# Kernel optimization log

Hardware: AMD Instinct MI355X
Metric: run time of the kernel (lower is better)

## Reference

```python
import jax, jax.numpy as jnp
import numpy as np

N_NODES = 100000
N_EDGES = 1600000
IN_CH, HID_CH, OUT_CH = 128, 64, 32


def setup_inputs() -> dict:
    key = jax.random.key(0)
    k1, k2, k3, k4 = jax.random.split(key, 4)
    x = jax.random.normal(k1, (N_NODES, IN_CH), dtype=jnp.float32)
    edge_index = jax.random.randint(k2, (2, N_EDGES), 0, N_NODES, dtype=jnp.int32)
    # Glorot-ish scaling like PyG's GCNConv init
    W1 = jax.random.normal(k3, (IN_CH, HID_CH), dtype=jnp.float32) / np.sqrt(IN_CH)
    b1 = jnp.zeros((HID_CH,), dtype=jnp.float32)
    W2 = jax.random.normal(k4, (HID_CH, OUT_CH), dtype=jnp.float32) / np.sqrt(HID_CH)
    b2 = jnp.zeros((OUT_CH,), dtype=jnp.float32)
    return {"x": x, "edge_index": edge_index, "W1": W1, "b1": b1, "W2": W2, "b2": b2}


def reference(x, edge_index, W1, b1, W2, b2):
    # PyG GCNConv semantics: add self-loops, symmetric deg^{-1/2} normalization,
    # linear transform, scatter-add aggregation to destination nodes, add bias.
    N = x.shape[0]
    loops = jnp.arange(N, dtype=edge_index.dtype)
    src = jnp.concatenate([edge_index[0], loops])  # [E+N]
    dst = jnp.concatenate([edge_index[1], loops])  # [E+N]

    deg = jax.ops.segment_sum(jnp.ones_like(src, dtype=x.dtype), dst, num_segments=N)
    dis = jnp.where(deg > 0, jax.lax.rsqrt(jnp.maximum(deg, 1.0)), 0.0)  # deg^{-1/2}
    norm = (dis[src] * dis[dst])[:, None]  # [E+N, 1]

    def gcn_conv(h, W, b):
        h = h @ W                                   # [N, C_out]
        msgs = h[src] * norm                        # gather + scale, [E+N, C_out]
        return jax.ops.segment_sum(msgs, dst, num_segments=N) + b

    h = jax.nn.relu(gcn_conv(x, W1, b1))
    # dropout is identity in eval mode (training=False)
    return gcn_conv(h, W2, b2)
```

## Files before the change

### kernel.cpp

```cpp
#include <hip/hip_runtime.h>
#include <hip/hip_bf16.h>

#define IN_CH 128
#define HID_CH 64
#define OUT_CH 32
#define EPB 2048
#define MAXB 512

typedef unsigned short ushort_t;
typedef __attribute__((ext_vector_type(8))) short short8;
typedef __attribute__((ext_vector_type(4))) float float4v;
typedef __attribute__((ext_vector_type(4))) float fx4;
typedef __attribute__((ext_vector_type(4))) unsigned ux4;
using half8 = __attribute__((ext_vector_type(8))) _Float16;

static __device__ __forceinline__ ushort_t f2bf(float f) {
    unsigned u = __float_as_uint(f);
    unsigned r = (u + 0x7fff + ((u >> 16) & 1)) >> 16;
    return (ushort_t)r;
}
static __device__ __forceinline__ float bf_lo(unsigned u) { return __uint_as_float(u << 16); }
static __device__ __forceinline__ float bf_hi(unsigned u) { return __uint_as_float(u & 0xffff0000u); }

static __device__ __forceinline__ unsigned f2h2(float lo, float hi) {
    union { _Float16 h[2]; unsigned u; } v;
    v.h[0] = (_Float16)lo;
    v.h[1] = (_Float16)hi;
    return v.u;
}
static __device__ __forceinline__ unsigned pkh(float a, float b) {
    auto p = __builtin_amdgcn_cvt_pkrtz(a, b);
    union { decltype(p) h; unsigned u; } v;
    v.h = p;
    return v.u;
}


__global__ __launch_bounds__(256) void k_partition(const int* __restrict__ src,
                                                   const int* __restrict__ dst,
                                                   int* __restrict__ gcursor,
                                                   unsigned* __restrict__ pairs,
                                                   int E, int nbk, int cap, int PB,
                                                   const float* __restrict__ W1,
                                                   const float* __restrict__ W2,
                                                   unsigned* __restrict__ wsW) {
    __shared__ int lhist[MAXB];
    __shared__ int lbase[MAXB];
    __shared__ int lcur[MAXB];
    const int tid = threadIdx.x;

    if (blockIdx.x >= PB) {
        int s = (blockIdx.x - PB) * 256 + tid;
        if (s < 1024) {
            int lane = s & 63;
            int nt = (s >> 6) & 3;
            int kc = s >> 8;
            int c = nt * 16 + (lane & 15);
            int k0 = kc * 32 + (lane >> 4) * 8;
            unsigned o[4];
#pragma unroll
            for (int d = 0; d < 4; ++d) {
                unsigned lo = f2bf(W1[(k0 + 2 * d) * 64 + c]);
                unsigned hi = f2bf(W1[(k0 + 2 * d + 1) * 64 + c]);
                o[d] = lo | (hi << 16);
            }
            ((uint4*)wsW)[s] = make_uint4(o[0], o[1], o[2], o[3]);
        } else {
            int q = s - 1024;
            int lane = q & 63;
            int f = q >> 6;
            int c = (f & 1) * 16 + (lane & 15);
            int k0 = (f >> 1) * 32 + (lane >> 4) * 8;
            unsigned o[4];
#pragma unroll
            for (int d = 0; d < 4; ++d)
                o[d] = f2h2(W2[(k0 + 2 * d) * 32 + c], W2[(k0 + 2 * d + 1) * 32 + c]);
            ((uint4*)wsW)[1024 + q] = make_uint4(o[0], o[1], o[2], o[3]);
        }
        return;
    }

    for (int b = tid; b < nbk; b += 256) { lhist[b] = 0; lcur[b] = 0; }
    __syncthreads();
    int s[8], d[8];
    const int e0 = blockIdx.x * EPB;
#pragma unroll
    for (int j = 0; j < 8; ++j) {
        int e = e0 + j * 256 + tid;
        if (e < E) {
            s[j] = src[e];
            d[j] = dst[e];
            atomicAdd(&lhist[d[j] >> 8], 1);
        } else {
            d[j] = -1;
        }
    }
    __syncthreads();
    for (int b = tid; b < nbk; b += 256)
        lbase[b] = lhist[b] ? atomicAdd(&gcursor[b], lhist[b]) : 0;
    __syncthreads();
#pragma unroll
    for (int j = 0; j < 8; ++j) {
        if (d[j] >= 0) {
            int b = d[j] >> 8;
            int loc = atomicAdd(&lcur[b], 1);
            int idx = lbase[b] + loc;
            if (idx < cap)
                pairs[(long long)b * cap + idx] = ((unsigned)s[j] << 8) | (unsigned)(d[j] & 255);
        }
    }
}


__global__ __launch_bounds__(256) void k_bucket_build(const unsigned* __restrict__ pairs,
                                                      const int* __restrict__ gcursor,
                                                      int* __restrict__ rowptr,
                                                      int* __restrict__ col,
                                                      float* __restrict__ dis,
                                                      unsigned* __restrict__ h1d,
                                                      int cap, int N) {
    __shared__ int lc[256];
    __shared__ int ls[256];
    __shared__ int lcur[256];
    const int b = blockIdx.x, tid = threadIdx.x;

    if (b == 0 && tid < 32)
        h1d[(long long)(tid >> 4) * (N + 1) * 16 + (long long)N * 16 + (tid & 15)] = 0;

    int ga = min(gcursor[2 * tid], cap);
    int gb = min(gcursor[2 * tid + 1], cap);
    ls[tid] = ga + gb;
    __syncthreads();
    for (int off = 1; off < 256; off <<= 1) {
        int val = (tid >= off) ? ls[tid - off] : 0;
        __syncthreads();
        ls[tid] += val;
        __syncthreads();
    }
    const int p = b >> 1;
    const int base = (p ? ls[p - 1] : 0) + ((b & 1) ? min(gcursor[b - 1], cap) : 0);
    const int total = ls[255];
    __syncthreads();
    if (b == 0 && tid == 0) rowptr[N] = total;

    lc[tid] = 0;
    __syncthreads();
    const int cnt = min(gcursor[b], cap);
    const unsigned* pp = pairs + (long long)b * cap;
    for (int i = tid; i < cnt; i += 256) atomicAdd(&lc[pp[i] & 255], 1);
    __syncthreads();
    const int v = lc[tid];
    ls[tid] = v;
    __syncthreads();
    for (int off = 1; off < 256; off <<= 1) {
        int val = (tid >= off) ? ls[tid - off] : 0;
        __syncthreads();
        ls[tid] += val;
        __syncthreads();
    }
    const int excl = ls[tid] - v;
    const int row = b * 256 + tid;
    if (row < N) {
        rowptr[row] = base + excl;
        dis[row] = rsqrtf((float)(v + 1));
    }
    lcur[tid] = base + excl;
    __syncthreads();
    for (int i = tid; i < cnt; i += 256) {
        unsigned pk = pp[i];
        int pos = atomicAdd(&lcur[pk & 255], 1);
        col[pos] = (int)(pk >> 8);
    }
}


__global__ __launch_bounds__(256) void k_mm1(const float* __restrict__ X,
                                             const unsigned* __restrict__ wsW,
                                             const float* __restrict__ dis,
                                             ushort_t* __restrict__ H, int N) {
    const int tid = threadIdx.x;
    const int wv = tid >> 6, lane = tid & 63;
    const int quad = lane >> 4, n16 = lane & 15;
    const int rowbase = blockIdx.x * 64 + wv * 16;
    const int myrow = rowbase + n16;
    const bool rok = (myrow < N);

    float4v acc0 = {}, acc1 = {}, acc2 = {}, acc3 = {};

#pragma unroll
    for (int kc = 0; kc < 4; ++kc) {
        float4 xa = make_float4(0.f, 0.f, 0.f, 0.f), xb = xa;
        if (rok) {
            const float4* p = (const float4*)(X + (long long)myrow * 128 + kc * 32 + quad * 8);
            xa = p[0];
            xb = p[1];
        }
        unsigned pk[4];
        pk[0] = (unsigned)f2bf(xa.x) | ((unsigned)f2bf(xa.y) << 16);
        pk[1] = (unsigned)f2bf(xa.z) | ((unsigned)f2bf(xa.w) << 16);
        pk[2] = (unsigned)f2bf(xb.x) | ((unsigned)f2bf(xb.y) << 16);
        pk[3] = (unsigned)f2bf(xb.z) | ((unsigned)f2bf(xb.w) << 16);
        short8 a;
        a[0] = (short)(pk[0] & 0xffff); a[1] = (short)(pk[0] >> 16);
        a[2] = (short)(pk[1] & 0xffff); a[3] = (short)(pk[1] >> 16);
        a[4] = (short)(pk[2] & 0xffff); a[5] = (short)(pk[2] >> 16);
        a[6] = (short)(pk[3] & 0xffff); a[7] = (short)(pk[3] >> 16);

        const short8* wb = (const short8*)wsW;
        short8 b0 = wb[(kc * 4 + 0) * 64 + lane];
        short8 b1 = wb[(kc * 4 + 1) * 64 + lane];
        short8 b2 = wb[(kc * 4 + 2) * 64 + lane];
        short8 b3 = wb[(kc * 4 + 3) * 64 + lane];

        acc0 = __builtin_amdgcn_mfma_f32_16x16x32_bf16(a, b0, acc0, 0, 0, 0);
        acc1 = __builtin_amdgcn_mfma_f32_16x16x32_bf16(a, b1, acc1, 0, 0, 0);
        acc2 = __builtin_amdgcn_mfma_f32_16x16x32_bf16(a, b2, acc2, 0, 0, 0);
        acc3 = __builtin_amdgcn_mfma_f32_16x16x32_bf16(a, b3, acc3, 0, 0, 0);
    }

    const long long hb1 = (long long)(N + 1) * 32;
#pragma unroll
    for (int i = 0; i < 4; ++i) {
        int row = rowbase + quad * 4 + i;
        if (row < N) {
            float dr = dis[row];
            long long o = (long long)row * 32 + n16;
            H[o]            = f2bf(dr * acc0[i]);
            H[o + 16]       = f2bf(dr * acc1[i]);
            H[hb1 + o]      = f2bf(dr * acc2[i]);
            H[hb1 + o + 16] = f2bf(dr * acc3[i]);
        }
    }
}


__global__ __launch_bounds__(256, 8) void k_gather1h(const unsigned* __restrict__ h,
                                                     const int* __restrict__ rowptr,
                                                     const int* __restrict__ col,
                                                     const float* __restrict__ dis,
                                                     const float* __restrict__ b1,
                                                     unsigned* __restrict__ z, int N) {
    const int tid = threadIdx.x;
    const int wv = tid >> 6, lane = tid & 63;
    const int t = lane & 3, g = lane >> 2;
    const int xcd = blockIdx.x & 7;
    const int hf = xcd >> 2;
    const int pb = ((blockIdx.x >> 3) << 2) | (xcd & 3);
    const int nwh = ((gridDim.x >> 3) << 2) * 4;

    const uint4* h4 = (const uint4*)h + (long long)hf * (N + 1) * 4;
    ux4* zp = (ux4*)z + (long long)hf * (N + 1) * 4;
    const float4 ba = ((const float4*)b1)[hf * 8 + t * 2];
    const float4 bb = ((const float4*)b1)[hf * 8 + t * 2 + 1];

    const int NBR = (N + 15) >> 4;

    for (int ri = pb * 4 + wv; ri < NBR; ri += nwh) {
        const int r0 = ri * 16;
        int rp_l = rowptr[min(r0 + min(lane, 16), N)];
        float dis_l = (lane < 16 && r0 + lane < N) ? dis[r0 + lane] : 0.f;
        const int sg = __shfl(rp_l, g);
        const int dg = __shfl(rp_l, g + 1) - sg;
        const float drg = __shfl(dis_l, g);
        const int rme = min(r0 + g, N);

        int mc0 = N, mc1 = N, mc2 = N, mc3 = N, mc4 = N, mc5 = N;
        if (t < dg)      mc0 = __builtin_nontemporal_load(col + sg + t);
        if (4 + t < dg)  mc1 = __builtin_nontemporal_load(col + sg + 4 + t);
        if (8 + t < dg)  mc2 = __builtin_nontemporal_load(col + sg + 8 + t);
        if (12 + t < dg) mc3 = __builtin_nontemporal_load(col + sg + 12 + t);
        if (16 + t < dg) mc4 = __builtin_nontemporal_load(col + sg + 16 + t);
        if (20 + t < dg) mc5 = __builtin_nontemporal_load(col + sg + 20 + t);

        uint4 us = h4[(long long)rme * 4 + t];
        float2 p0 = make_float2(bf_lo(us.x), bf_hi(us.x));
        float2 p1 = make_float2(bf_lo(us.y), bf_hi(us.y));
        float2 p2 = make_float2(bf_lo(us.z), bf_hi(us.z));
        float2 p3 = make_float2(bf_lo(us.w), bf_hi(us.w));

#define GATH(MC, J)                                                   \
    {                                                                 \
        int s_ = __shfl((MC), (g << 2) + (J));                        \
        uint4 uu = h4[(long long)s_ * 4 + t];                         \
        p0 += make_float2(bf_lo(uu.x), bf_hi(uu.x));                  \
        p1 += make_float2(bf_lo(uu.y), bf_hi(uu.y));                  \
        p2 += make_float2(bf_lo(uu.z), bf_hi(uu.z));                  \
        p3 += make_float2(bf_lo(uu.w), bf_hi(uu.w));                  \
    }
#pragma unroll
        for (int j = 0; j < 4; ++j) GATH(mc0, j)
#pragma unroll
        for (int j = 0; j < 4; ++j) GATH(mc1, j)
#pragma unroll
        for (int j = 0; j < 4; ++j) GATH(mc2, j)
#pragma unroll
        for (int j = 0; j < 4; ++j) GATH(mc3, j)
#pragma unroll
        for (int j = 0; j < 4; ++j) GATH(mc4, j)
#pragma unroll
        for (int j = 0; j < 4; ++j) GATH(mc5, j)
        if (__any(dg > 24)) {
            int mc6 = N, mc7 = N;
            if (24 + t < dg) mc6 = __builtin_nontemporal_load(col + sg + 24 + t);
            if (28 + t < dg) mc7 = __builtin_nontemporal_load(col + sg + 28 + t);
#pragma unroll
            for (int j = 0; j < 4; ++j) GATH(mc6, j)
#pragma unroll
            for (int j = 0; j < 4; ++j) GATH(mc7, j)
        }
        for (int u = 32;; ++u) {
            bool act = u < dg;
            if (!__any(act)) break;
            if (act) {
                int s_ = col[sg + u];
                uint4 uu = h4[(long long)s_ * 4 + t];
                p0 += make_float2(bf_lo(uu.x), bf_hi(uu.x));
                p1 += make_float2(bf_lo(uu.y), bf_hi(uu.y));
                p2 += make_float2(bf_lo(uu.z), bf_hi(uu.z));
                p3 += make_float2(bf_lo(uu.w), bf_hi(uu.w));
            }
        }
#undef GATH

        if (r0 + g < N) {
            float z0 = fmaxf(fmaf(drg, p0.x, ba.x), 0.f);
            float z1 = fmaxf(fmaf(drg, p0.y, ba.y), 0.f);
            float z2 = fmaxf(fmaf(drg, p1.x, ba.z), 0.f);
            float z3 = fmaxf(fmaf(drg, p1.y, ba.w), 0.f);
            float z4 = fmaxf(fmaf(drg, p2.x, bb.x), 0.f);
            float z5 = fmaxf(fmaf(drg, p2.y, bb.y), 0.f);
            float z6 = fmaxf(fmaf(drg, p3.x, bb.z), 0.f);
            float z7 = fmaxf(fmaf(drg, p3.y, bb.w), 0.f);
            ux4 zo;
            zo.x = pkh(z0, z1);
            zo.y = pkh(z2, z3);
            zo.z = pkh(z4, z5);
            zo.w = pkh(z6, z7);
            __builtin_nontemporal_store(zo, zp + (long long)(r0 + g) * 4 + t);
        }
    }
}


__global__ __launch_bounds__(256) void k_mm2(const unsigned* __restrict__ z,
                                             const unsigned* __restrict__ wsW2,
                                             const float* __restrict__ dis,
                                             ushort_t* __restrict__ H2, int N) {
    const int tid = threadIdx.x;
    if (blockIdx.x == 0 && tid < 16)
        ((unsigned*)H2)[(long long)(tid >> 3) * (N + 1) * 8 + (long long)N * 8 + (tid & 7)] = 0;

    const int wv = tid >> 6, lane = tid & 63;
    const int n16 = lane & 15, kq = lane >> 4;
    const int rowbase = blockIdx.x * 64 + wv * 16;
    const int rz = min(rowbase + n16, N - 1);

    const uint4* z4 = (const uint4*)z;
    uint4 a0 = z4[(long long)rz * 4 + kq];
    uint4 a1 = z4[(long long)(N + 1) * 4 + (long long)rz * 4 + kq];

    const half8* wfh = (const half8*)wsW2;
    const half8 bf00 = wfh[lane];
    const half8 bf01 = wfh[64 + lane];
    const half8 bf10 = wfh[128 + lane];
    const half8 bf11 = wfh[192 + lane];

    union U { uint4 u; half8 h; };
    U ua0, ua1;
    ua0.u = a0;
    ua1.u = a1;

    float4v c0 = {}, c1 = {};
    c0 = __builtin_amdgcn_mfma_f32_16x16x32_f16(ua0.h, bf00, c0, 0, 0, 0);
    c0 = __builtin_amdgcn_mfma_f32_16x16x32_f16(ua1.h, bf10, c0, 0, 0, 0);
    c1 = __builtin_amdgcn_mfma_f32_16x16x32_f16(ua0.h, bf01, c1, 0, 0, 0);
    c1 = __builtin_amdgcn_mfma_f32_16x16x32_f16(ua1.h, bf11, c1, 0, 0, 0);

    float dis_l = (lane < 16 && rowbase + lane < N) ? dis[rowbase + lane] : 0.f;
    const long long hb1 = (long long)(N + 1) * 16;
#pragma unroll
    for (int i = 0; i < 4; ++i) {
        int rr = rowbase + kq * 4 + i;
        float dr = __shfl(dis_l, kq * 4 + i);
        if (rr < N) {
            H2[(long long)rr * 16 + n16]       = f2bf(dr * c0[i]);
            H2[hb1 + (long long)rr * 16 + n16] = f2bf(dr * c1[i]);
        }
    }
}


__global__ __launch_bounds__(256, 8) void k_agg32h(const unsigned* __restrict__ h2,
                                                   const int* __restrict__ rowptr,
                                                   const int* __restrict__ col,
                                                   const float* __restrict__ dis,
                                                   const float* __restrict__ b2,
                                                   float* __restrict__ out, int N) {
    const int tid = threadIdx.x;
    const int wv = tid >> 6, lane = tid & 63;
    const int t = lane & 3, g = lane >> 2;
    const int xcd = blockIdx.x & 7;
    const int hf = xcd >> 2;
    const int pb = ((blockIdx.x >> 3) << 2) | (xcd & 3);
    const int nwh = ((gridDim.x >> 3) << 2) * 4;

    const uint2* hw = (const uint2*)h2 + (long long)hf * (N + 1) * 4;
    const float4 bq = ((const float4*)b2)[hf * 4 + t];

    const int NBR = (N + 15) >> 4;

    for (int ri = pb * 4 + wv; ri < NBR; ri += nwh) {
        const int r0 = ri * 16;
        int rp_l = rowptr[min(r0 + min(lane, 16), N)];
        float dis_l = (lane < 16 && r0 + lane < N) ? dis[r0 + lane] : 0.f;
        const int sg = __shfl(rp_l, g);
        const int dg = __shfl(rp_l, g + 1) - sg;
        const float drg = __shfl(dis_l, g);
        const int rme = min(r0 + g, N);

        int mc0 = N, mc1 = N, mc2 = N, mc3 = N, mc4 = N, mc5 = N;
        if (t < dg)      mc0 = __builtin_nontemporal_load(col + sg + t);
        if (4 + t < dg)  mc1 = __builtin_nontemporal_load(col + sg + 4 + t);
        if (8 + t < dg)  mc2 = __builtin_nontemporal_load(col + sg + 8 + t);
        if (12 + t < dg) mc3 = __builtin_nontemporal_load(col + sg + 12 + t);
        if (16 + t < dg) mc4 = __builtin_nontemporal_load(col + sg + 16 + t);
        if (20 + t < dg) mc5 = __builtin_nontemporal_load(col + sg + 20 + t);

        uint2 us = hw[(long long)rme * 4 + t];
        float2 p0 = make_float2(bf_lo(us.x), bf_hi(us.x));
        float2 p1 = make_float2(bf_lo(us.y), bf_hi(us.y));

#define GATH2(MC, J)                                                  \
    {                                                                 \
        int s_ = __shfl((MC), (g << 2) + (J));                        \
        uint2 uu = hw[(long long)s_ * 4 + t];                         \
        p0 += make_float2(bf_lo(uu.x), bf_hi(uu.x));                  \
        p1 += make_float2(bf_lo(uu.y), bf_hi(uu.y));                  \
    }
#pragma unroll
        for (int j = 0; j < 4; ++j) GATH2(mc0, j)
#pragma unroll
        for (int j = 0; j < 4; ++j) GATH2(mc1, j)
#pragma unroll
        for (int j = 0; j < 4; ++j) GATH2(mc2, j)
#pragma unroll
        for (int j = 0; j < 4; ++j) GATH2(mc3, j)
#pragma unroll
        for (int j = 0; j < 4; ++j) GATH2(mc4, j)
#pragma unroll
        for (int j = 0; j < 4; ++j) GATH2(mc5, j)
        if (__any(dg > 24)) {
            int mc6 = N, mc7 = N;
            if (24 + t < dg) mc6 = __builtin_nontemporal_load(col + sg + 24 + t);
            if (28 + t < dg) mc7 = __builtin_nontemporal_load(col + sg + 28 + t);
#pragma unroll
            for (int j = 0; j < 4; ++j) GATH2(mc6, j)
#pragma unroll
            for (int j = 0; j < 4; ++j) GATH2(mc7, j)
        }
        for (int u = 32;; ++u) {
            bool act = u < dg;
            if (!__any(act)) break;
            if (act) {
                int s_ = col[sg + u];
                uint2 uu = hw[(long long)s_ * 4 + t];
                p0 += make_float2(bf_lo(uu.x), bf_hi(uu.x));
                p1 += make_float2(bf_lo(uu.y), bf_hi(uu.y));
            }
        }
#undef GATH2

        if (r0 + g < N) {
            fx4 o;
            o.x = bq.x + drg * p0.x;
            o.y = bq.y + drg * p0.y;
            o.z = bq.z + drg * p1.x;
            o.w = bq.w + drg * p1.y;
            fx4* op = (fx4*)(out + (long long)(r0 + g) * 32 + hf * 16 + t * 4);
            __builtin_nontemporal_store(o, op);
        }
    }
}

extern "C" void kernel_launch(void* const* d_in, const int* in_sizes, int n_in,
                              void* d_out, int out_size, void* d_ws, size_t ws_size,
                              hipStream_t stream) {
    const float* x  = (const float*)d_in[0];
    const int*   ei = (const int*)d_in[1];
    const float* W1 = (const float*)d_in[2];
    const float* b1 = (const float*)d_in[3];
    const float* W2 = (const float*)d_in[4];
    const float* b2 = (const float*)d_in[5];
    float* out = (float*)d_out;

    const int N = in_sizes[0] / IN_CH;
    const int E = in_sizes[1] / 2;
    const int* esrc = ei;
    const int* edst = ei + E;

    int nbk = (N + 255) >> 8;
    if (nbk > MAXB) nbk = MAXB;
    const int per_b = (E + nbk - 1) / nbk;
    const int cap = per_b + per_b / 4 + 256;

    int* rowptr   = (int*)d_ws;
    int* gcursor  = rowptr + (((N + 1) + 15) & ~15);
    unsigned* wsW = (unsigned*)(gcursor + MAXB);
    int* col      = (int*)(wsW + 5120);
    float* dis    = (float*)(col + ((E + 15) & ~15));
    ushort_t* h1  = (ushort_t*)(dis + ((N + 15) & ~15));
    unsigned* scratch = (unsigned*)(h1 + (((long long)(N + 1) * 64 + 31) & ~31LL));
    unsigned* pairs = scratch;
    unsigned* z     = scratch;
    ushort_t* h2    = h1;

    const int B = 256;
    const int PB = (E + EPB - 1) / EPB;
    const int NBR = (N + 15) >> 4;
    int bph = (NBR + 7) / 8;
    int agg_blocks = ((2 * bph + 7) / 8) * 8;
    if (agg_blocks > 2048) agg_blocks = 2048;

    hipMemsetAsync(gcursor, 0, MAXB * sizeof(int), stream);
    k_partition<<<PB + 5, B, 0, stream>>>(esrc, edst, gcursor, pairs, E, nbk, cap, PB, W1, W2, wsW);
    k_bucket_build<<<nbk, B, 0, stream>>>(pairs, gcursor, rowptr, col, dis, (unsigned*)h1, cap, N);

    k_mm1<<<(N + 63) / 64, B, 0, stream>>>(x, wsW, dis, h1, N);

    k_gather1h<<<agg_blocks, B, 0, stream>>>((const unsigned*)h1, rowptr, col, dis, b1, z, N);

    k_mm2<<<(N + 63) / 64, B, 0, stream>>>(z, wsW + 4096, dis, h2, N);

    k_agg32h<<<agg_blocks, B, 0, stream>>>((const unsigned*)h2, rowptr, col, dis, b2, out, N);
}
```

Baseline: 232.7 us.

## Split layer-1 hidden features into four 16-channel quarters mapped to XCD pairs

Changes the h1 and z layouts from two 32-channel halves to four 16-channel quarters. Each pair of XCDs now gathers only its quarter, so the gathered working set per XCD's L2 shrinks and is more likely to stay cache-resident. mm1, bucket_build's sentinel zeroing and mm2's loads are updated to match the new layout. The trade-off is twice as many index loads and shuffles per feature byte, smaller 8-byte gathers, and a fixed 2048-block grid for the gather.

```diff
diff --git a/kernel.cpp b/kernel.cpp
--- a/kernel.cpp
+++ b/kernel.cpp
@@ -12,6 +12,7 @@
 typedef __attribute__((ext_vector_type(4))) float float4v;
 typedef __attribute__((ext_vector_type(4))) float fx4;
 typedef __attribute__((ext_vector_type(4))) unsigned ux4;
+typedef __attribute__((ext_vector_type(2))) unsigned ux2;
 using half8 = __attribute__((ext_vector_type(8))) _Float16;
 
 static __device__ __forceinline__ ushort_t f2bf(float f) {
@@ -125,7 +126,7 @@
     const int b = blockIdx.x, tid = threadIdx.x;
 
     if (b == 0 && tid < 32)
-        h1d[(long long)(tid >> 4) * (N + 1) * 16 + (long long)N * 16 + (tid & 15)] = 0;
+        h1d[(long long)(tid >> 3) * (N + 1) * 8 + (long long)N * 8 + (tid & 7)] = 0;
 
     int ga = min(gcursor[2 * tid], cap);
     int gb = min(gcursor[2 * tid + 1], cap);
@@ -218,23 +219,23 @@
         acc3 = __builtin_amdgcn_mfma_f32_16x16x32_bf16(a, b3, acc3, 0, 0, 0);
     }
 
-    const long long hb1 = (long long)(N + 1) * 32;
+    const long long qs = (long long)(N + 1) * 16;
 #pragma unroll
     for (int i = 0; i < 4; ++i) {
         int row = rowbase + quad * 4 + i;
         if (row < N) {
             float dr = dis[row];
-            long long o = (long long)row * 32 + n16;
-            H[o]            = f2bf(dr * acc0[i]);
-            H[o + 16]       = f2bf(dr * acc1[i]);
-            H[hb1 + o]      = f2bf(dr * acc2[i]);
-            H[hb1 + o + 16] = f2bf(dr * acc3[i]);
-        }
-    }
-}
-
-
-__global__ __launch_bounds__(256, 8) void k_gather1h(const unsigned* __restrict__ h,
+            long long o = (long long)row * 16 + n16;
+            H[o]          = f2bf(dr * acc0[i]);
+            H[qs + o]     = f2bf(dr * acc1[i]);
+            H[2 * qs + o] = f2bf(dr * acc2[i]);
+            H[3 * qs + o] = f2bf(dr * acc3[i]);
+        }
+    }
+}
+
+
+__global__ __launch_bounds__(256, 8) void k_gather1q(const unsigned* __restrict__ h,
                                                      const int* __restrict__ rowptr,
                                                      const int* __restrict__ col,
                                                      const float* __restrict__ dis,
@@ -244,14 +245,13 @@
     const int wv = tid >> 6, lane = tid & 63;
     const int t = lane & 3, g = lane >> 2;
     const int xcd = blockIdx.x & 7;
-    const int hf = xcd >> 2;
-    const int pb = ((blockIdx.x >> 3) << 2) | (xcd & 3);
-    const int nwh = ((gridDim.x >> 3) << 2) * 4;
-
-    const uint4* h4 = (const uint4*)h + (long long)hf * (N + 1) * 4;
-    ux4* zp = (ux4*)z + (long long)hf * (N + 1) * 4;
-    const float4 ba = ((const float4*)b1)[hf * 8 + t * 2];
-    const float4 bb = ((const float4*)b1)[hf * 8 + t * 2 + 1];
+    const int qf = xcd >> 1;
+    const int pb = ((blockIdx.x >> 3) << 1) | (xcd & 1);
+    const int nwh = ((gridDim.x >> 3) << 1) * 4;
+
+    const uint2* hq = (const uint2*)h + (long long)qf * (N + 1) * 4;
+    ux2* zq = (ux2*)z + (long long)qf * (N + 1) * 4;
+    const float4 bq = ((const float4*)b1)[qf * 4 + t];
 
     const int NBR = (N + 15) >> 4;
 
@@ -272,71 +272,59 @@
         if (16 + t < dg) mc4 = __builtin_nontemporal_load(col + sg + 16 + t);
         if (20 + t < dg) mc5 = __builtin_nontemporal_load(col + sg + 20 + t);
 
-        uint4 us = h4[(long long)rme * 4 + t];
+        uint2 us = hq[(long long)rme * 4 + t];
         float2 p0 = make_float2(bf_lo(us.x), bf_hi(us.x));
         float2 p1 = make_float2(bf_lo(us.y), bf_hi(us.y));
-        float2 p2 = make_float2(bf_lo(us.z), bf_hi(us.z));
-        float2 p3 = make_float2(bf_lo(us.w), bf_hi(us.w));
-
-#define GATH(MC, J)                                                   \
+
+#define GATQ(MC, J)                                                   \
     {                                                                 \
         int s_ = __shfl((MC), (g << 2) + (J));                        \
-        uint4 uu = h4[(long long)s_ * 4 + t];                         \
+        uint2 uu = hq[(long long)s_ * 4 + t];                         \
         p0 += make_float2(bf_lo(uu.x), bf_hi(uu.x));                  \
         p1 += make_float2(bf_lo(uu.y), bf_hi(uu.y));                  \
-        p2 += make_float2(bf_lo(uu.z), bf_hi(uu.z));                  \
-        p3 += make_float2(bf_lo(uu.w), bf_hi(uu.w));                  \
-    }
-#pragma unroll
-        for (int j = 0; j < 4; ++j) GATH(mc0, j)
-#pragma unroll
-        for (int j = 0; j < 4; ++j) GATH(mc1, j)
-#pragma unroll
-        for (int j = 0; j < 4; ++j) GATH(mc2, j)
-#pragma unroll
-        for (int j = 0; j < 4; ++j) GATH(mc3, j)
-#pragma unroll
-        for (int j = 0; j < 4; ++j) GATH(mc4, j)
-#pragma unroll
-        for (int j = 0; j < 4; ++j) GATH(mc5, j)
+    }
+#pragma unroll
+        for (int j = 0; j < 4; ++j) GATQ(mc0, j)
+#pragma unroll
+        for (int j = 0; j < 4; ++j) GATQ(mc1, j)
+#pragma unroll
+        for (int j = 0; j < 4; ++j) GATQ(mc2, j)
+#pragma unroll
+        for (int j = 0; j < 4; ++j) GATQ(mc3, j)
+#pragma unroll
+        for (int j = 0; j < 4; ++j) GATQ(mc4, j)
+#pragma unroll
+        for (int j = 0; j < 4; ++j) GATQ(mc5, j)
         if (__any(dg > 24)) {
             int mc6 = N, mc7 = N;
             if (24 + t < dg) mc6 = __builtin_nontemporal_load(col + sg + 24 + t);
             if (28 + t < dg) mc7 = __builtin_nontemporal_load(col + sg + 28 + t);
 #pragma unroll
-            for (int j = 0; j < 4; ++j) GATH(mc6, j)
-#pragma unroll
-            for (int j = 0; j < 4; ++j) GATH(mc7, j)
+            for (int j = 0; j < 4; ++j) GATQ(mc6, j)
+#pragma unroll
+            for (int j = 0; j < 4; ++j) GATQ(mc7, j)
         }
         for (int u = 32;; ++u) {
             bool act = u < dg;
             if (!__any(act)) break;
             if (act) {
                 int s_ = col[sg + u];
-                uint4 uu = h4[(long long)s_ * 4 + t];
+                uint2 uu = hq[(long long)s_ * 4 + t];
                 p0 += make_float2(bf_lo(uu.x), bf_hi(uu.x));
                 p1 += make_float2(bf_lo(uu.y), bf_hi(uu.y));
-                p2 += make_float2(bf_lo(uu.z), bf_hi(uu.z));
-                p3 += make_float2(bf_lo(uu.w), bf_hi(uu.w));
             }
         }
-#undef GATH
+#undef GATQ
 
         if (r0 + g < N) {
-            float z0 = fmaxf(fmaf(drg, p0.x, ba.x), 0.f);
-            float z1 = fmaxf(fmaf(drg, p0.y, ba.y), 0.f);
-            float z2 = fmaxf(fmaf(drg, p1.x, ba.z), 0.f);
-            float z3 = fmaxf(fmaf(drg, p1.y, ba.w), 0.f);
-            float z4 = fmaxf(fmaf(drg, p2.x, bb.x), 0.f);
-            float z5 = fmaxf(fmaf(drg, p2.y, bb.y), 0.f);
-            float z6 = fmaxf(fmaf(drg, p3.x, bb.z), 0.f);
-            float z7 = fmaxf(fmaf(drg, p3.y, bb.w), 0.f);
-            ux4 zo;
+            float z0 = fmaxf(fmaf(drg, p0.x, bq.x), 0.f);
+            float z1 = fmaxf(fmaf(drg, p0.y, bq.y), 0.f);
+            float z2 = fmaxf(fmaf(drg, p1.x, bq.z), 0.f);
+            float z3 = fmaxf(fmaf(drg, p1.y, bq.w), 0.f);
+            ux2 zo;
             zo.x = pkh(z0, z1);
             zo.y = pkh(z2, z3);
-            zo.z = pkh(z4, z5);
-            zo.w = pkh(z6, z7);
-            __builtin_nontemporal_store(zo, zp + (long long)(r0 + g) * 4 + t);
+            __builtin_nontemporal_store(zo, zq + (long long)(r0 + g) * 4 + t);
         }
     }
 }
@@ -356,8 +344,9 @@
     const int rz = min(rowbase + n16, N - 1);
 
     const uint4* z4 = (const uint4*)z;
-    uint4 a0 = z4[(long long)rz * 4 + kq];
-    uint4 a1 = z4[(long long)(N + 1) * 4 + (long long)rz * 4 + kq];
+    const long long qreg = (long long)(N + 1) * 2;
+    uint4 a0 = z4[(long long)(kq >> 1) * qreg + (long long)rz * 2 + (kq & 1)];
+    uint4 a1 = z4[(long long)(2 + (kq >> 1)) * qreg + (long long)rz * 2 + (kq & 1)];
 
     const half8* wfh = (const half8*)wsW2;
     const half8 bf00 = wfh[lane];
@@ -517,6 +506,7 @@
     const int B = 256;
     const int PB = (E + EPB - 1) / EPB;
     const int NBR = (N + 15) >> 4;
+    const int g1_blocks = 2048;
     int bph = (NBR + 7) / 8;
     int agg_blocks = ((2 * bph + 7) / 8) * 8;
     if (agg_blocks > 2048) agg_blocks = 2048;
@@ -527,7 +517,7 @@
 
     k_mm1<<<(N + 63) / 64, B, 0, stream>>>(x, wsW, dis, h1, N);
 
-    k_gather1h<<<agg_blocks, B, 0, stream>>>((const unsigned*)h1, rowptr, col, dis, b1, z, N);
+    k_gather1q<<<g1_blocks, B, 0, stream>>>((const unsigned*)h1, rowptr, col, dis, b1, z, N);
 
     k_mm2<<<(N + 63) / 64, B, 0, stream>>>(z, wsW + 4096, dis, h2, N);
 
```

Measured after the change: 248.7 us. 6.9% more time.

## Replace bucketed two-pass CSR build with degree count, scan, and atomic scatter

Applied to the files above, without the earlier changes.

The CSR construction no longer partitions edges into 256-node buckets with a per-bucket LDS sort. It now counts in-degrees with global atomics, runs a two-kernel exclusive scan over nodes to produce rowptr and dis, and scatters source ids into col using per-node atomic cursors. This drops the intermediate pairs buffer and its extra read and write pass, but adds two kernel launches and 3.2M global atomics spread across random addresses. Edge order within a row becomes nondeterministic.

```diff
diff --git a/kernel.cpp b/kernel.cpp
--- a/kernel.cpp
+++ b/kernel.cpp
@@ -5,7 +5,6 @@
 #define HID_CH 64
 #define OUT_CH 32
 #define EPB 2048
-#define MAXB 512
 
 typedef unsigned short ushort_t;
 typedef __attribute__((ext_vector_type(8))) short short8;
@@ -36,21 +35,15 @@
 }
 
 
-__global__ __launch_bounds__(256) void k_partition(const int* __restrict__ src,
-                                                   const int* __restrict__ dst,
-                                                   int* __restrict__ gcursor,
-                                                   unsigned* __restrict__ pairs,
-                                                   int E, int nbk, int cap, int PB,
-                                                   const float* __restrict__ W1,
-                                                   const float* __restrict__ W2,
-                                                   unsigned* __restrict__ wsW) {
-    __shared__ int lhist[MAXB];
-    __shared__ int lbase[MAXB];
-    __shared__ int lcur[MAXB];
-    const int tid = threadIdx.x;
-
-    if (blockIdx.x >= PB) {
-        int s = (blockIdx.x - PB) * 256 + tid;
+__global__ __launch_bounds__(256) void k_deg(const int* __restrict__ dst,
+                                             int* __restrict__ cursor,
+                                             int E, int DB,
+                                             const float* __restrict__ W1,
+                                             const float* __restrict__ W2,
+                                             unsigned* __restrict__ wsW) {
+    const int tid = threadIdx.x;
+    if (blockIdx.x >= DB) {
+        int s = (blockIdx.x - DB) * 256 + tid;
         if (s < 1024) {
             int lane = s & 63;
             int nt = (s >> 6) & 3;
@@ -80,56 +73,72 @@
         return;
     }
 
-    for (int b = tid; b < nbk; b += 256) { lhist[b] = 0; lcur[b] = 0; }
-    __syncthreads();
-    int s[8], d[8];
     const int e0 = blockIdx.x * EPB;
 #pragma unroll
     for (int j = 0; j < 8; ++j) {
         int e = e0 + j * 256 + tid;
-        if (e < E) {
-            s[j] = src[e];
-            d[j] = dst[e];
-            atomicAdd(&lhist[d[j] >> 8], 1);
-        } else {
-            d[j] = -1;
-        }
-    }
+        if (e < E) atomicAdd(&cursor[__builtin_nontemporal_load(dst + e)], 1);
+    }
+}
+
+
+__global__ __launch_bounds__(256) void k_scanA(const int* __restrict__ cursor,
+                                               int* __restrict__ bsum, int N) {
+    __shared__ int ls[256];
+    const int tid = threadIdx.x;
+    const int base = blockIdx.x * 2048;
+    int s = 0;
+#pragma unroll
+    for (int i = 0; i < 8; ++i) {
+        int r = base + i * 256 + tid;
+        s += (r < N) ? cursor[r] : 0;
+    }
+    ls[tid] = s;
     __syncthreads();
-    for (int b = tid; b < nbk; b += 256)
-        lbase[b] = lhist[b] ? atomicAdd(&gcursor[b], lhist[b]) : 0;
-    __syncthreads();
-#pragma unroll
-    for (int j = 0; j < 8; ++j) {
-        if (d[j] >= 0) {
-            int b = d[j] >> 8;
-            int loc = atomicAdd(&lcur[b], 1);
-            int idx = lbase[b] + loc;
-            if (idx < cap)
-                pairs[(long long)b * cap + idx] = ((unsigned)s[j] << 8) | (unsigned)(d[j] & 255);
-        }
-    }
-}
-
-
-__global__ __launch_bounds__(256) void k_bucket_build(const unsigned* __restrict__ pairs,
-                                                      const int* __restrict__ gcursor,
-                                                      int* __restrict__ rowptr,
-                                                      int* __restrict__ col,
-                                                      float* __restrict__ dis,
-                                                      unsigned* __restrict__ h1d,
-                                                      int cap, int N) {
-    __shared__ int lc[256];
+    for (int off = 128; off; off >>= 1) {
+        if (tid < off) ls[tid] += ls[tid + off];
+        __syncthreads();
+    }
+    if (tid == 0) bsum[blockIdx.x] = ls[0];
+}
+
+
+__global__ __launch_bounds__(256) void k_scanB(int* __restrict__ cursor,
+                                               const int* __restrict__ bsum,
+                                               int* __restrict__ rowptr,
+                                               float* __restrict__ dis,
+                                               unsigned* __restrict__ h1d,
+                                               int N, int E) {
+    __shared__ int ldeg[2048];
     __shared__ int ls[256];
-    __shared__ int lcur[256];
-    const int b = blockIdx.x, tid = threadIdx.x;
+    __shared__ int gbase_s;
+    const int tid = threadIdx.x, b = blockIdx.x;
 
     if (b == 0 && tid < 32)
         h1d[(long long)(tid >> 4) * (N + 1) * 16 + (long long)N * 16 + (tid & 15)] = 0;
-
-    int ga = min(gcursor[2 * tid], cap);
-    int gb = min(gcursor[2 * tid + 1], cap);
-    ls[tid] = ga + gb;
+    if (b == 0 && tid == 0) rowptr[N] = E;
+
+    if (tid == 0) {
+        int g = 0;
+        for (int i = 0; i < b; ++i) g += bsum[i];
+        gbase_s = g;
+    }
+    const int base = b * 2048;
+#pragma unroll
+    for (int i = 0; i < 8; ++i) {
+        int r = base + i * 256 + tid;
+        ldeg[i * 256 + tid] = (r < N) ? cursor[r] : 0;
+    }
+    __syncthreads();
+
+    int loc[8];
+    int s = 0;
+#pragma unroll
+    for (int i = 0; i < 8; ++i) {
+        loc[i] = s;
+        s += ldeg[tid * 8 + i];
+    }
+    ls[tid] = s;
     __syncthreads();
     for (int off = 1; off < 256; off <<= 1) {
         int val = (tid >= off) ? ls[tid - off] : 0;
@@ -137,39 +146,35 @@
         ls[tid] += val;
         __syncthreads();
     }
-    const int p = b >> 1;
-    const int base = (p ? ls[p - 1] : 0) + ((b & 1) ? min(gcursor[b - 1], cap) : 0);
-    const int total = ls[255];
-    __syncthreads();
-    if (b == 0 && tid == 0) rowptr[N] = total;
-
-    lc[tid] = 0;
-    __syncthreads();
-    const int cnt = min(gcursor[b], cap);
-    const unsigned* pp = pairs + (long long)b * cap;
-    for (int i = tid; i < cnt; i += 256) atomicAdd(&lc[pp[i] & 255], 1);
-    __syncthreads();
-    const int v = lc[tid];
-    ls[tid] = v;
-    __syncthreads();
-    for (int off = 1; off < 256; off <<= 1) {
-        int val = (tid >= off) ? ls[tid - off] : 0;
-        __syncthreads();
-        ls[tid] += val;
-        __syncthreads();
-    }
-    const int excl = ls[tid] - v;
-    const int row = b * 256 + tid;
-    if (row < N) {
-        rowptr[row] = base + excl;
-        dis[row] = rsqrtf((float)(v + 1));
-    }
-    lcur[tid] = base + excl;
-    __syncthreads();
-    for (int i = tid; i < cnt; i += 256) {
-        unsigned pk = pp[i];
-        int pos = atomicAdd(&lcur[pk & 255], 1);
-        col[pos] = (int)(pk >> 8);
+    const int texcl = (tid ? ls[tid - 1] : 0) + gbase_s;
+#pragma unroll
+    for (int i = 0; i < 8; ++i) {
+        int r = base + tid * 8 + i;
+        if (r < N) {
+            int start = texcl + loc[i];
+            rowptr[r] = start;
+            cursor[r] = start;
+            dis[r] = rsqrtf((float)(ldeg[tid * 8 + i] + 1));
+        }
+    }
+}
+
+
+__global__ __launch_bounds__(256) void k_scatter(const int* __restrict__ src,
+                                                 const int* __restrict__ dst,
+                                                 int* __restrict__ cursor,
+                                                 int* __restrict__ col, int E) {
+    const int tid = threadIdx.x;
+    const int e0 = blockIdx.x * EPB;
+#pragma unroll
+    for (int j = 0; j < 8; ++j) {
+        int e = e0 + j * 256 + tid;
+        if (e < E) {
+            int d = __builtin_nontemporal_load(dst + e);
+            int s = __builtin_nontemporal_load(src + e);
+            int pos = atomicAdd(&cursor[d], 1);
+            col[pos] = s;
+        }
     }
 }
 
@@ -498,32 +503,31 @@
     const int* esrc = ei;
     const int* edst = ei + E;
 
-    int nbk = (N + 255) >> 8;
-    if (nbk > MAXB) nbk = MAXB;
-    const int per_b = (E + nbk - 1) / nbk;
-    const int cap = per_b + per_b / 4 + 256;
-
     int* rowptr   = (int*)d_ws;
-    int* gcursor  = rowptr + (((N + 1) + 15) & ~15);
-    unsigned* wsW = (unsigned*)(gcursor + MAXB);
+    int* cursor   = rowptr + (((N + 1) + 15) & ~15);
+    int* bsum     = cursor + ((N + 15) & ~15);
+    unsigned* wsW = (unsigned*)(bsum + 64);
     int* col      = (int*)(wsW + 5120);
     float* dis    = (float*)(col + ((E + 15) & ~15));
     ushort_t* h1  = (ushort_t*)(dis + ((N + 15) & ~15));
     unsigned* scratch = (unsigned*)(h1 + (((long long)(N + 1) * 64 + 31) & ~31LL));
-    unsigned* pairs = scratch;
     unsigned* z     = scratch;
     ushort_t* h2    = h1;
 
     const int B = 256;
-    const int PB = (E + EPB - 1) / EPB;
-    const int NBR = (N + 15) >> 4;
-    int bph = (NBR + 7) / 8;
+    const int DB = (E + EPB - 1) / EPB;
+    const int SB = (N + 2047) / 2048;
+    const int NBR16 = (N + 15) >> 4;
+    int bph = (NBR16 + 7) / 8;
     int agg_blocks = ((2 * bph + 7) / 8) * 8;
     if (agg_blocks > 2048) agg_blocks = 2048;
 
-    hipMemsetAsync(gcursor, 0, MAXB * sizeof(int), stream);
-    k_partition<<<PB + 5, B, 0, stream>>>(esrc, edst, gcursor, pairs, E, nbk, cap, PB, W1, W2, wsW);
-    k_bucket_build<<<nbk, B, 0, stream>>>(pairs, gcursor, rowptr, col, dis, (unsigned*)h1, cap, N);
+    hipMemsetAsync(cursor, 0, (size_t)N * sizeof(int), stream);
+
+    k_deg<<<DB + 5, B, 0, stream>>>(edst, cursor, E, DB, W1, W2, wsW);
+    k_scanA<<<SB, B, 0, stream>>>(cursor, bsum, N);
+    k_scanB<<<SB, B, 0, stream>>>(cursor, bsum, rowptr, dis, (unsigned*)h1, N, E);
+    k_scatter<<<DB, B, 0, stream>>>(esrc, edst, cursor, col, E);
 
     k_mm1<<<(N + 63) / 64, B, 0, stream>>>(x, wsW, dis, h1, N);
 
```

New measurement: 406.5 us. +74.7%, slower.

## Store H2 interleaved per row and aggregate all 32 channels per row group

Applied to the files above, without the earlier changes.

The second-layer features were stored as two half-planes of 16 channels, and the aggregation split work between XCD groups by half. H2 is now written row-contiguous (32 bf16 per row), and the aggregation kernel uses 8 lanes per row, so each gathered neighbour row is one 64-byte contiguous read. This halves the number of col/rowptr reads and shuffles per edge. In exchange it gives up the per-XCD L2 locality of each half-plane, and the grid is fixed at 2048 blocks.

```diff
diff --git a/kernel.cpp b/kernel.cpp
--- a/kernel.cpp
+++ b/kernel.cpp
@@ -348,7 +348,7 @@
                                              ushort_t* __restrict__ H2, int N) {
     const int tid = threadIdx.x;
     if (blockIdx.x == 0 && tid < 16)
-        ((unsigned*)H2)[(long long)(tid >> 3) * (N + 1) * 8 + (long long)N * 8 + (tid & 7)] = 0;
+        ((unsigned*)H2)[(long long)N * 16 + tid] = 0;
 
     const int wv = tid >> 6, lane = tid & 63;
     const int n16 = lane & 15, kq = lane >> 4;
@@ -377,107 +377,85 @@
     c1 = __builtin_amdgcn_mfma_f32_16x16x32_f16(ua1.h, bf11, c1, 0, 0, 0);
 
     float dis_l = (lane < 16 && rowbase + lane < N) ? dis[rowbase + lane] : 0.f;
-    const long long hb1 = (long long)(N + 1) * 16;
 #pragma unroll
     for (int i = 0; i < 4; ++i) {
         int rr = rowbase + kq * 4 + i;
         float dr = __shfl(dis_l, kq * 4 + i);
         if (rr < N) {
-            H2[(long long)rr * 16 + n16]       = f2bf(dr * c0[i]);
-            H2[hb1 + (long long)rr * 16 + n16] = f2bf(dr * c1[i]);
-        }
-    }
-}
-
-
-__global__ __launch_bounds__(256, 8) void k_agg32h(const unsigned* __restrict__ h2,
-                                                   const int* __restrict__ rowptr,
-                                                   const int* __restrict__ col,
-                                                   const float* __restrict__ dis,
-                                                   const float* __restrict__ b2,
-                                                   float* __restrict__ out, int N) {
+            H2[(long long)rr * 32 + n16]      = f2bf(dr * c0[i]);
+            H2[(long long)rr * 32 + 16 + n16] = f2bf(dr * c1[i]);
+        }
+    }
+}
+
+
+__global__ __launch_bounds__(256, 8) void k_agg32(const unsigned* __restrict__ h,
+                                                  const int* __restrict__ rowptr,
+                                                  const int* __restrict__ col,
+                                                  const float* __restrict__ dis,
+                                                  const float* __restrict__ b,
+                                                  float* __restrict__ out, int N) {
     const int tid = threadIdx.x;
     const int wv = tid >> 6, lane = tid & 63;
-    const int t = lane & 3, g = lane >> 2;
-    const int xcd = blockIdx.x & 7;
-    const int hf = xcd >> 2;
-    const int pb = ((blockIdx.x >> 3) << 2) | (xcd & 3);
-    const int nwh = ((gridDim.x >> 3) << 2) * 4;
-
-    const uint2* hw = (const uint2*)h2 + (long long)hf * (N + 1) * 4;
-    const float4 bq = ((const float4*)b2)[hf * 4 + t];
-
-    const int NBR = (N + 15) >> 4;
-
-    for (int ri = pb * 4 + wv; ri < NBR; ri += nwh) {
-        const int r0 = ri * 16;
-        int rp_l = rowptr[min(r0 + min(lane, 16), N)];
-        float dis_l = (lane < 16 && r0 + lane < N) ? dis[r0 + lane] : 0.f;
+    const int t = lane & 7, g = lane >> 3;
+    const float4 bq = ((const float4*)b)[t];
+    const uint2* hw = (const uint2*)h;
+    const int NB = (N + 7) >> 3;
+    const int step = gridDim.x * 4;
+
+    for (int rb = blockIdx.x * 4 + wv; rb < NB; rb += step) {
+        const int r0 = rb * 8;
+        int rp_l = rowptr[min(r0 + min(lane, 8), N)];
+        float dis_l = (lane < 8 && r0 + lane < N) ? dis[r0 + lane] : 0.f;
         const int sg = __shfl(rp_l, g);
         const int dg = __shfl(rp_l, g + 1) - sg;
         const float drg = __shfl(dis_l, g);
+
+        int mc1 = N, mc2 = N, mc3 = N;
+        if (t < dg)      mc1 = __builtin_nontemporal_load(col + sg + t);
+        if (8 + t < dg)  mc2 = __builtin_nontemporal_load(col + sg + 8 + t);
+        if (16 + t < dg) mc3 = __builtin_nontemporal_load(col + sg + 16 + t);
+
         const int rme = min(r0 + g, N);
-
-        int mc0 = N, mc1 = N, mc2 = N, mc3 = N, mc4 = N, mc5 = N;
-        if (t < dg)      mc0 = __builtin_nontemporal_load(col + sg + t);
-        if (4 + t < dg)  mc1 = __builtin_nontemporal_load(col + sg + 4 + t);
-        if (8 + t < dg)  mc2 = __builtin_nontemporal_load(col + sg + 8 + t);
-        if (12 + t < dg) mc3 = __builtin_nontemporal_load(col + sg + 12 + t);
-        if (16 + t < dg) mc4 = __builtin_nontemporal_load(col + sg + 16 + t);
-        if (20 + t < dg) mc5 = __builtin_nontemporal_load(col + sg + 20 + t);
-
-        uint2 us = hw[(long long)rme * 4 + t];
+        uint2 us = hw[(long long)rme * 8 + t];
         float2 p0 = make_float2(bf_lo(us.x), bf_hi(us.x));
         float2 p1 = make_float2(bf_lo(us.y), bf_hi(us.y));
 
-#define GATH2(MC, J)                                                  \
+#define GAT2(MC, U)                                                   \
     {                                                                 \
-        int s_ = __shfl((MC), (g << 2) + (J));                        \
-        uint2 uu = hw[(long long)s_ * 4 + t];                         \
+        int s_ = __shfl((MC), (g << 3) + (U));                        \
+        uint2 uu = hw[(long long)s_ * 8 + t];                         \
         p0 += make_float2(bf_lo(uu.x), bf_hi(uu.x));                  \
         p1 += make_float2(bf_lo(uu.y), bf_hi(uu.y));                  \
     }
 #pragma unroll
-        for (int j = 0; j < 4; ++j) GATH2(mc0, j)
-#pragma unroll
-        for (int j = 0; j < 4; ++j) GATH2(mc1, j)
-#pragma unroll
-        for (int j = 0; j < 4; ++j) GATH2(mc2, j)
-#pragma unroll
-        for (int j = 0; j < 4; ++j) GATH2(mc3, j)
-#pragma unroll
-        for (int j = 0; j < 4; ++j) GATH2(mc4, j)
-#pragma unroll
-        for (int j = 0; j < 4; ++j) GATH2(mc5, j)
+        for (int u = 0; u < 8; ++u) GAT2(mc1, u)
+#pragma unroll
+        for (int u = 0; u < 8; ++u) GAT2(mc2, u)
+#pragma unroll
+        for (int u = 0; u < 8; ++u) GAT2(mc3, u)
         if (__any(dg > 24)) {
-            int mc6 = N, mc7 = N;
-            if (24 + t < dg) mc6 = __builtin_nontemporal_load(col + sg + 24 + t);
-            if (28 + t < dg) mc7 = __builtin_nontemporal_load(col + sg + 28 + t);
-#pragma unroll
-            for (int j = 0; j < 4; ++j) GATH2(mc6, j)
-#pragma unroll
-            for (int j = 0; j < 4; ++j) GATH2(mc7, j)
-        }
-        for (int u = 32;; ++u) {
-            bool act = u < dg;
-            if (!__any(act)) break;
-            if (act) {
-                int s_ = col[sg + u];
-                uint2 uu = hw[(long long)s_ * 4 + t];
-                p0 += make_float2(bf_lo(uu.x), bf_hi(uu.x));
-                p1 += make_float2(bf_lo(uu.y), bf_hi(uu.y));
-            }
-        }
-#undef GATH2
-
-        if (r0 + g < N) {
+            int mc4 = N;
+            if (24 + t < dg) mc4 = __builtin_nontemporal_load(col + sg + 24 + t);
+#pragma unroll
+            for (int u = 0; u < 8; ++u) GAT2(mc4, u)
+        }
+        for (int u = 32; u < dg; ++u) {
+            int s_ = col[sg + u];
+            uint2 uu = hw[(long long)s_ * 8 + t];
+            p0 += make_float2(bf_lo(uu.x), bf_hi(uu.x));
+            p1 += make_float2(bf_lo(uu.y), bf_hi(uu.y));
+        }
+#undef GAT2
+
+        const int rr = r0 + g;
+        if (rr < N) {
             fx4 o;
             o.x = bq.x + drg * p0.x;
             o.y = bq.y + drg * p0.y;
             o.z = bq.z + drg * p1.x;
             o.w = bq.w + drg * p1.y;
-            fx4* op = (fx4*)(out + (long long)(r0 + g) * 32 + hf * 16 + t * 4);
-            __builtin_nontemporal_store(o, op);
+            __builtin_nontemporal_store(o, (fx4*)(out + (long long)rr * 32 + t * 4));
         }
     }
 }
@@ -516,10 +494,10 @@
 
     const int B = 256;
     const int PB = (E + EPB - 1) / EPB;
-    const int NBR = (N + 15) >> 4;
-    int bph = (NBR + 7) / 8;
-    int agg_blocks = ((2 * bph + 7) / 8) * 8;
-    if (agg_blocks > 2048) agg_blocks = 2048;
+    const int NBR16 = (N + 15) >> 4;
+    int bph = (NBR16 + 7) / 8;
+    int g1_blocks = ((2 * bph + 7) / 8) * 8;
+    if (g1_blocks > 2048) g1_blocks = 2048;
 
     hipMemsetAsync(gcursor, 0, MAXB * sizeof(int), stream);
     k_partition<<<PB + 5, B, 0, stream>>>(esrc, edst, gcursor, pairs, E, nbk, cap, PB, W1, W2, wsW);
@@ -527,9 +505,9 @@
 
     k_mm1<<<(N + 63) / 64, B, 0, stream>>>(x, wsW, dis, h1, N);
 
-    k_gather1h<<<agg_blocks, B, 0, stream>>>((const unsigned*)h1, rowptr, col, dis, b1, z, N);
+    k_gather1h<<<g1_blocks, B, 0, stream>>>((const unsigned*)h1, rowptr, col, dis, b1, z, N);
 
     k_mm2<<<(N + 63) / 64, B, 0, stream>>>(z, wsW + 4096, dis, h2, N);
 
-    k_agg32h<<<agg_blocks, B, 0, stream>>>((const unsigned*)h2, rowptr, col, dis, b2, out, N);
-}
+    k_agg32<<<2048, B, 0, stream>>>((const unsigned*)h2, rowptr, col, dis, b2, out, N);
+}
```

Measured after the change: 232.7 us. Within noise of the previous version (+0.0%).
